# Optimization experiments

Measured on AMD Instinct MI355X. Metric: run time of the kernel, lower is better.

The kernel has to match this reference:

```python
import jax, jax.numpy as jnp
import numpy as np

B, S, D = 1, 4096, 512
H, DK, DV = 8, 64, 64


def setup_inputs() -> dict:
    key = jax.random.key(0)
    ks = jax.random.split(key, 8)
    s = 1.0 / np.sqrt(D)
    return {
        "queries": jax.random.normal(ks[0], (B, S, D), jnp.float32),
        "keys": jax.random.normal(ks[1], (B, S, D), jnp.float32),
        "values": jax.random.normal(ks[2], (B, S, D), jnp.float32),
        # Linear weights stored as [in, out] for x @ W
        "Wq": jax.random.normal(ks[3], (D, H * DK), jnp.float32) * s,
        "Wk": jax.random.normal(ks[4], (D, H * DK), jnp.float32) * s,
        "Wv": jax.random.normal(ks[5], (D, H * DV), jnp.float32) * s,
        "Wo": jax.random.normal(ks[6], (H * DV, D), jnp.float32) * s,
        "bo": jax.random.normal(ks[7], (D,), jnp.float32) * 0.02,
    }


def reference(queries, keys, values, Wq, Wk, Wv, Wo, bo):
    b, qlen = values.shape[0], queries.shape[1]
    q = (queries @ Wq).reshape(b, qlen, H, DK)
    k = (keys @ Wk).reshape(b, keys.shape[1], H, DK)
    v = (values @ Wv).reshape(b, values.shape[1], H, DV)
    scale = DK ** 0.5
    # naive full attention: materialize [b, h, sq, sk] scores
    scores = jnp.einsum("bqhd,bkhd->bhqk", q, k) / scale
    attn = jax.nn.softmax(scores, axis=-1)
    out = jnp.einsum("bhqk,bkhd->bqhd", attn, v).reshape(b, qlen, H * DV)
    out = out @ Wo + bo          # first fc_out
    out = out @ Wo + bo          # second fc_out (module applies it twice when not reversible)
    return out
```

## Files before the change

kernel.cpp:

```cpp
#include <hip/hip_runtime.h>

#define S_LEN  4096
#define DMODEL 512
#define NH     8
#define HD     64

typedef _Float16 f16x8 __attribute__((ext_vector_type(8)));
typedef _Float16 f16x4 __attribute__((ext_vector_type(4)));
typedef float    f32x4 __attribute__((ext_vector_type(4)));

static __device__ __forceinline__ unsigned short f2h(float x) {
  return __builtin_bit_cast(unsigned short, (_Float16)x);
}

__global__ __launch_bounds__(256) void wtrans_kernel(
    const float* __restrict__ w0, const float* __restrict__ w1,
    const float* __restrict__ w2, const float* __restrict__ w3,
    unsigned short* __restrict__ o0, unsigned short* __restrict__ o1,
    unsigned short* __restrict__ o2, unsigned short* __restrict__ o3,
    unsigned short* __restrict__ o3s)
{
  __shared__ unsigned short T[64 * 72];
  const float* W; unsigned short* O;
  switch (blockIdx.z) {
    case 0:  W = w0; O = o0; break;
    case 1:  W = w1; O = o1; break;
    case 2:  W = w2; O = o2; break;
    default: W = w3; O = o3; break;
  }
  const int tid = threadIdx.x;
  const int k0 = blockIdx.x * 64, n0 = blockIdx.y * 64;
  const int c4 = (tid & 15) * 4;
#pragma unroll
  for (int rp = 0; rp < 4; ++rp) {
    int r = rp * 16 + (tid >> 4);
    float4 x = *(const float4*)(W + (k0 + r) * DMODEL + n0 + c4);
    T[(c4 + 0) * 72 + r] = f2h(x.x);
    T[(c4 + 1) * 72 + r] = f2h(x.y);
    T[(c4 + 2) * 72 + r] = f2h(x.z);
    T[(c4 + 3) * 72 + r] = f2h(x.w);
    if (blockIdx.z == 3) {
      f16x4 st;
      st[0] = (_Float16)x.x; st[1] = (_Float16)x.y;
      st[2] = (_Float16)x.z; st[3] = (_Float16)x.w;
      *(f16x4*)&o3s[(k0 + r) * DMODEL + n0 + c4] = st;
    }
  }
  __syncthreads();
#pragma unroll
  for (int it = 0; it < 2; ++it) {
    int i = tid + it * 256;
    int nl = i >> 3, c = i & 7;
    *(f16x8*)&O[(n0 + nl) * DMODEL + k0 + c * 8] = *(const f16x8*)&T[nl * 72 + c * 8];
  }
}

__global__ __launch_bounds__(256) void gemm_kernel(
    const void* __restrict__ A0, const void* __restrict__ A1,
    const void* __restrict__ A2, const void* __restrict__ A3,
    const unsigned short* __restrict__ B0, const unsigned short* __restrict__ B1,
    const unsigned short* __restrict__ B2, const unsigned short* __restrict__ B3,
    void* __restrict__ C0, void* __restrict__ C1,
    void* __restrict__ C2, void* __restrict__ C3,
    const float* __restrict__ bias, unsigned short* __restrict__ vtg,
    const float* __restrict__ wo_f32, const float* __restrict__ bo_in,
    float* __restrict__ bo2_out,
    int a_fp32_mask, int c_fp32_mask)
{
  constexpr int K = DMODEL, N = DMODEL;
  __shared__ unsigned short As[64 * 32];
  __shared__ unsigned short Bs[64 * 32];
  const int z = blockIdx.z;
  if (z == 3 && blockIdx.x >= 8) {
    if (blockIdx.x < 16 && blockIdx.y == 0 && wo_f32) {
      int col = (blockIdx.x - 8) * 64 + (threadIdx.x & 63);
      float s = bo_in[col];
#pragma unroll 8
      for (int j = 0; j < DMODEL; ++j) s = fmaf(bo_in[j], wo_f32[j * DMODEL + col], s);
      bo2_out[col] = s;
    }
    return;
  }
  const void* Av; const unsigned short* Bt; void* Cv;
  switch (z) {
    case 0:  Av = A0; Bt = B0; Cv = C0; break;
    case 1:  Av = A1; Bt = B1; Cv = C1; break;
    case 2:  Av = A2; Bt = B2; Cv = C2; break;
    default: Av = A3; Bt = B3; Cv = C3; break;
  }
  const int a_fp32 = (a_fp32_mask >> z) & 1;
  const int c_fp32 = (c_fp32_mask >> z) & 1;
  const int tid  = threadIdx.x;
  const int lane = tid & 63;
  const int wid  = tid >> 6;
  const int quad = lane >> 4, l16 = lane & 15;
  const int m0 = blockIdx.x * 64, n0 = blockIdx.y * 64;
  const int wm = (wid >> 1) * 32, wn = (wid & 1) * 32;
  const int r  = tid >> 2, ck = (tid & 3) * 8;
  f32x4 acc[2][2] = {};

  for (int k0 = 0; k0 < K; k0 += 32) {
    __syncthreads();
    if (a_fp32) {
      const float* p = (const float*)Av + (m0 + r) * K + k0 + ck;
      float4 x = *(const float4*)p;
      float4 y = *(const float4*)(p + 4);
      f16x8 av;
      av[0] = (_Float16)x.x; av[1] = (_Float16)x.y;
      av[2] = (_Float16)x.z; av[3] = (_Float16)x.w;
      av[4] = (_Float16)y.x; av[5] = (_Float16)y.y;
      av[6] = (_Float16)y.z; av[7] = (_Float16)y.w;
      *(f16x8*)&As[r * 32 + ck] = av;
    } else {
      *(f16x8*)&As[r * 32 + ck] =
          *(const f16x8*)((const unsigned short*)Av + (m0 + r) * K + k0 + ck);
    }
    *(f16x8*)&Bs[r * 32 + ck] = *(const f16x8*)(Bt + (n0 + r) * K + k0 + ck);
    __syncthreads();

    f16x8 a0 = *(const f16x8*)&As[(wm + l16) * 32 + quad * 8];
    f16x8 a1 = *(const f16x8*)&As[(wm + 16 + l16) * 32 + quad * 8];
    f16x8 b0 = *(const f16x8*)&Bs[(wn + l16) * 32 + quad * 8];
    f16x8 b1 = *(const f16x8*)&Bs[(wn + 16 + l16) * 32 + quad * 8];
    acc[0][0] = __builtin_amdgcn_mfma_f32_16x16x32_f16(a0, b0, acc[0][0], 0, 0, 0);
    acc[0][1] = __builtin_amdgcn_mfma_f32_16x16x32_f16(a0, b1, acc[0][1], 0, 0, 0);
    acc[1][0] = __builtin_amdgcn_mfma_f32_16x16x32_f16(a1, b0, acc[1][0], 0, 0, 0);
    acc[1][1] = __builtin_amdgcn_mfma_f32_16x16x32_f16(a1, b1, acc[1][1], 0, 0, 0);
  }

  const int do_vt = (vtg != nullptr) && (z == 2);
#pragma unroll
  for (int mt = 0; mt < 2; ++mt)
#pragma unroll
    for (int nt = 0; nt < 2; ++nt) {
      int col = n0 + wn + nt * 16 + l16;
      float bv = bias ? bias[col] : 0.f;
#pragma unroll
      for (int g = 0; g < 4; ++g) {
        int row = m0 + wm + mt * 16 + quad * 4 + g;
        float val = acc[mt][nt][g] + bv;
        if (do_vt)        vtg[col * S_LEN + row] = f2h(val);
        else if (c_fp32)  ((float*)Cv)[row * N + col] = val;
        else              ((unsigned short*)Cv)[row * N + col] = f2h(val);
      }
    }
}

__global__ __launch_bounds__(256) void attn_kernel(
    const unsigned short* __restrict__ Qb, const unsigned short* __restrict__ Kb,
    const unsigned short* __restrict__ VtG,
    float* __restrict__ P0, unsigned short* __restrict__ P1,
    float* __restrict__ mp, float* __restrict__ lp)
{
  __shared__ unsigned short Ks[2][64 * 72];
  __shared__ unsigned short Vt[2 * 64 * 64];
  __shared__ float Msc[2][2][16];
  __shared__ float Lsc[2][2][16];

  const int tid  = threadIdx.x;
  const int lane = tid & 63;
  const int wid  = tid >> 6;
  const int qp   = wid & 1;
  const int kh   = wid >> 1;
  const int quad = lane >> 4, l16 = lane & 15;
  const int qb = blockIdx.x, h = blockIdx.y, z = blockIdx.z;
  const int hc = h * HD;
  const int qbase = qb * 64 + qp * 32;
  const int kz = z * 2048;

  f16x8 bq[2][2];
#pragma unroll
  for (int s = 0; s < 2; ++s) {
    int qrow = qbase + s * 16 + l16;
    bq[s][0] = *(const f16x8*)(Qb + qrow * DMODEL + hc + quad * 8);
    bq[s][1] = *(const f16x8*)(Qb + qrow * DMODEL + hc + 32 + quad * 8);
  }

  f32x4 o[2][4] = {};
  float m_run[2] = {-1e30f, -1e30f}, l_run[2] = {0.f, 0.f};

  f16x8 kreg[4], vreg[4];
#pragma unroll
  for (int it = 0; it < 4; ++it) {
    int s = it * 256 + tid;
    int khs = s >> 9, n = (s >> 3) & 63, c = s & 7;
    kreg[it] = *(const f16x8*)(Kb + (kz + khs * 1024 + n) * DMODEL + hc + c * 8);
    vreg[it] = *(const f16x8*)(VtG + (hc + n) * S_LEN + kz + khs * 1024 + c * 8);
  }

  for (int kbi = 0; kbi < 16; ++kbi) {
    __syncthreads();
#pragma unroll
    for (int it = 0; it < 4; ++it) {
      int s = it * 256 + tid;
      int khs = s >> 9, n = (s >> 3) & 63, c = s & 7;
      *(f16x8*)&Ks[khs][n * 72 + c * 8] = kreg[it];
      int vbase = (khs * 64 + n) * 16;
      int n15 = n & 15;
      f16x4 lo = __builtin_shufflevector(vreg[it], vreg[it], 0, 1, 2, 3);
      f16x4 hi = __builtin_shufflevector(vreg[it], vreg[it], 4, 5, 6, 7);
      *(f16x4*)&Vt[(vbase + ((2 * c) ^ n15)) * 4]     = lo;
      *(f16x4*)&Vt[(vbase + ((2 * c + 1) ^ n15)) * 4] = hi;
    }
    __syncthreads();

    if (kbi + 1 < 16) {
      int kb1 = (kbi + 1) * 64;
#pragma unroll
      for (int it = 0; it < 4; ++it) {
        int s = it * 256 + tid;
        int khs = s >> 9, n = (s >> 3) & 63, c = s & 7;
        kreg[it] = *(const f16x8*)(Kb + (kz + khs * 1024 + kb1 + n) * DMODEL + hc + c * 8);
        vreg[it] = *(const f16x8*)(VtG + (hc + n) * S_LEN + kz + khs * 1024 + kb1 + c * 8);
      }
    }

    f32x4 sT[2][4];
#pragma unroll
    for (int kt = 0; kt < 4; ++kt) {
      f16x8 ak0 = *(const f16x8*)&Ks[kh][(kt * 16 + l16) * 72 + quad * 8];
      f16x8 ak1 = *(const f16x8*)&Ks[kh][(kt * 16 + l16) * 72 + 32 + quad * 8];
#pragma unroll
      for (int s = 0; s < 2; ++s) {
        f32x4 a = {};
        a = __builtin_amdgcn_mfma_f32_16x16x32_f16(ak0, bq[s][0], a, 0, 0, 0);
        a = __builtin_amdgcn_mfma_f32_16x16x32_f16(ak1, bq[s][1], a, 0, 0, 0);
        sT[s][kt] = a;
      }
    }

    f16x4 pa[2][4];
#pragma unroll
    for (int s = 0; s < 2; ++s) {
      float vmax = -1e30f;
#pragma unroll
      for (int kt = 0; kt < 4; ++kt)
#pragma unroll
        for (int g = 0; g < 4; ++g) vmax = fmaxf(vmax, sT[s][kt][g]);
      vmax = fmaxf(vmax, __shfl_xor(vmax, 16));
      vmax = fmaxf(vmax, __shfl_xor(vmax, 32));

      if (__all(vmax <= m_run[s] + 8.0f)) {
        const float mn = m_run[s];
        float rs = 0.f;
#pragma unroll
        for (int kt = 0; kt < 4; ++kt)
#pragma unroll
          for (int g = 0; g < 4; ++g) {
            float p = __expf((sT[s][kt][g] - mn) * 0.125f);
            rs += p;
            pa[s][kt][g] = (_Float16)p;
          }
        rs += __shfl_xor(rs, 16);
        rs += __shfl_xor(rs, 32);
        l_run[s] += rs;
      } else {
        const float mn = fmaxf(m_run[s], vmax);
        const float alpha = __expf((m_run[s] - mn) * 0.125f);
        m_run[s] = mn;

        float rs = 0.f;
#pragma unroll
        for (int kt = 0; kt < 4; ++kt)
#pragma unroll
          for (int g = 0; g < 4; ++g) {
            float p = __expf((sT[s][kt][g] - mn) * 0.125f);
            rs += p;
            pa[s][kt][g] = (_Float16)p;
          }
        rs += __shfl_xor(rs, 16);
        rs += __shfl_xor(rs, 32);
        l_run[s] = l_run[s] * alpha + rs;

        float ag[4];
#pragma unroll
        for (int g = 0; g < 4; ++g) ag[g] = __shfl(alpha, quad * 4 + g);
#pragma unroll
        for (int nt = 0; nt < 4; ++nt)
#pragma unroll
          for (int g = 0; g < 4; ++g) o[s][nt][g] *= ag[g];
      }
    }

#pragma unroll
    for (int nt = 0; nt < 4; ++nt) {
      int dbase = (kh * 64 + nt * 16 + l16) * 16;
#pragma unroll
      for (int kt = 0; kt < 4; ++kt) {
        f16x4 bv = *(const f16x4*)&Vt[(dbase + ((kt * 4 + quad) ^ l16)) * 4];
#pragma unroll
        for (int s = 0; s < 2; ++s)
          o[s][nt] = __builtin_amdgcn_mfma_f32_16x16x16f16(pa[s][kt], bv, o[s][nt], 0, 0, 0);
      }
    }
  }

  __syncthreads();
  _Float16* Osc = (_Float16*)&Ks[0][0];
  if (kh == 1) {
#pragma unroll
    for (int s = 0; s < 2; ++s) {
      if (quad == 0) { Msc[qp][s][l16] = m_run[s]; Lsc[qp][s][l16] = l_run[s]; }
#pragma unroll
      for (int nt = 0; nt < 4; ++nt)
#pragma unroll
        for (int g = 0; g < 4; ++g)
          Osc[(qp * 64 + lane) * 32 + s * 16 + nt * 4 + g] = (_Float16)o[s][nt][g];
    }
  }
  __syncthreads();
  if (kh == 0) {
#pragma unroll
    for (int s = 0; s < 2; ++s) {
      const float m1 = Msc[qp][s][l16];
      const float l1 = Lsc[qp][s][l16];
      const float m  = fmaxf(m_run[s], m1);
      const float a0 = __expf((m_run[s] - m) * 0.125f);
      const float a1 = __expf((m1 - m) * 0.125f);
      const float lt = l_run[s] * a0 + l1 * a1;
      const float rl = 1.f / lt;
      if (quad == 0) {
        int q = qbase + s * 16 + l16;
        mp[(z * NH + h) * S_LEN + q] = m;
        lp[(z * NH + h) * S_LEN + q] = lt;
      }
      float a0g[4], a1g[4], rlg[4];
#pragma unroll
      for (int g = 0; g < 4; ++g) {
        a0g[g] = __shfl(a0, quad * 4 + g);
        a1g[g] = __shfl(a1, quad * 4 + g);
        rlg[g] = __shfl(rl, quad * 4 + g);
      }
#pragma unroll
      for (int g = 0; g < 4; ++g) {
        int row = qbase + s * 16 + quad * 4 + g;
#pragma unroll
        for (int nt = 0; nt < 4; ++nt) {
          float om = o[s][nt][g] * a0g[g] + (float)Osc[(qp * 64 + lane) * 32 + s * 16 + nt * 4 + g] * a1g[g];
          float val = om * rlg[g];
          if (z == 0) P0[row * DMODEL + hc + nt * 16 + l16] = val;
          else        P1[row * DMODEL + hc + nt * 16 + l16] = f2h(val);
        }
      }
    }
  }
}

__global__ __launch_bounds__(256) void merge_kernel(
    const float* __restrict__ P0, const unsigned short* __restrict__ P1,
    const float* __restrict__ mp, const float* __restrict__ lp,
    unsigned short* __restrict__ Ob)
{
  const int tid = threadIdx.x;
  const int qb = blockIdx.x, h = blockIdx.y;
  const int q = qb * 64 + (tid >> 2), hc = h * HD;
  const int dq = (tid & 3) * 16;
  const float m0 = mp[h * S_LEN + q],        l0 = lp[h * S_LEN + q];
  const float m1 = mp[(NH + h) * S_LEN + q], l1 = lp[(NH + h) * S_LEN + q];
  const float M  = fmaxf(m0, m1);
  float w0 = l0 * __expf((m0 - M) * 0.125f);
  float w1 = l1 * __expf((m1 - M) * 0.125f);
  const float rw = 1.f / (w0 + w1);
  w0 *= rw; w1 *= rw;
  const int base = q * DMODEL + hc + dq;
  f16x8 p1a = *(const f16x8*)&P1[base];
  f16x8 p1b = *(const f16x8*)&P1[base + 8];
  float4 x0 = *(const float4*)&P0[base];
  float4 x1 = *(const float4*)&P0[base + 4];
  float4 x2 = *(const float4*)&P0[base + 8];
  float4 x3 = *(const float4*)&P0[base + 12];
  f16x8 oa, ob;
  oa[0] = (_Float16)(w0 * x0.x + w1 * (float)p1a[0]);
  oa[1] = (_Float16)(w0 * x0.y + w1 * (float)p1a[1]);
  oa[2] = (_Float16)(w0 * x0.z + w1 * (float)p1a[2]);
  oa[3] = (_Float16)(w0 * x0.w + w1 * (float)p1a[3]);
  oa[4] = (_Float16)(w0 * x1.x + w1 * (float)p1a[4]);
  oa[5] = (_Float16)(w0 * x1.y + w1 * (float)p1a[5]);
  oa[6] = (_Float16)(w0 * x1.z + w1 * (float)p1a[6]);
  oa[7] = (_Float16)(w0 * x1.w + w1 * (float)p1a[7]);
  ob[0] = (_Float16)(w0 * x2.x + w1 * (float)p1b[0]);
  ob[1] = (_Float16)(w0 * x2.y + w1 * (float)p1b[1]);
  ob[2] = (_Float16)(w0 * x2.z + w1 * (float)p1b[2]);
  ob[3] = (_Float16)(w0 * x2.w + w1 * (float)p1b[3]);
  ob[4] = (_Float16)(w0 * x3.x + w1 * (float)p1b[4]);
  ob[5] = (_Float16)(w0 * x3.y + w1 * (float)p1b[5]);
  ob[6] = (_Float16)(w0 * x3.z + w1 * (float)p1b[6]);
  ob[7] = (_Float16)(w0 * x3.w + w1 * (float)p1b[7]);
  *(f16x8*)&Ob[base]     = oa;
  *(f16x8*)&Ob[base + 8] = ob;
}

extern "C" void kernel_launch(void* const* d_in, const int* in_sizes, int n_in,
                              void* d_out, int out_size, void* d_ws, size_t ws_size,
                              hipStream_t stream) {
  const float* q  = (const float*)d_in[0];
  const float* k  = (const float*)d_in[1];
  const float* v  = (const float*)d_in[2];
  const float* Wq = (const float*)d_in[3];
  const float* Wk = (const float*)d_in[4];
  const float* Wv = (const float*)d_in[5];
  const float* Wo = (const float*)d_in[6];
  const float* bo = (const float*)d_in[7];

  unsigned short* ws   = (unsigned short*)d_ws;
  unsigned short* Wqt  = ws;
  unsigned short* Wkt  = Wqt  + 262144;
  unsigned short* Wvt  = Wkt  + 262144;
  unsigned short* Wot  = Wvt  + 262144;
  unsigned short* Wof  = Wot  + 262144;
  unsigned short* Wo2t = Wof  + 262144;
  unsigned short* Qb   = Wo2t + 262144;
  unsigned short* Kb   = Qb   + 2097152;
  unsigned short* VtG  = Kb   + 2097152;
  unsigned short* Ab   = VtG  + 2097152;
  float*          bo2  = (float*)(Ab + 2097152);
  float*          mp   = bo2 + 512;
  float*          lp   = mp + 65536;

  wtrans_kernel<<<dim3(8, 8, 4), 256, 0, stream>>>(
      Wq, Wk, Wv, Wo, Wqt, Wkt, Wvt, Wot, Wof);

  gemm_kernel<<<dim3(64, 8, 4), 256, 0, stream>>>(
      q, k, v, Wot, Wqt, Wkt, Wvt, Wof, Qb, Kb, nullptr, Wo2t,
      nullptr, VtG, Wo, bo, bo2, 0x7, 0x0);

  attn_kernel<<<dim3(64, 8, 2), 256, 0, stream>>>(
      Qb, Kb, VtG, (float*)d_out, Ab, mp, lp);

  merge_kernel<<<dim3(64, 8), 256, 0, stream>>>(
      (const float*)d_out, Ab, mp, lp, Ab);

  gemm_kernel<<<dim3(64, 8, 1), 256, 0, stream>>>(
      Ab, nullptr, nullptr, nullptr, Wo2t, nullptr, nullptr, nullptr,
      d_out, nullptr, nullptr, nullptr, bo2, nullptr,
      nullptr, nullptr, nullptr, 0x0, 0x1);
}
```

Measured before the change: 213.6 us.

## Enlarge GEMM tiles to 128x128 and register-prefetch next K slice

The projection and output GEMMs move from 64x64 to 128x128 block tiles, with each wave computing a 4x4 grid of 16x16 MFMA tiles instead of 2x2. Global loads for the next K slice are issued into registers before the current slice's MFMAs, so memory latency overlaps with compute. This raises reuse of each shared-memory fragment and cuts redundant global reads. In exchange it uses more registers and launches far fewer blocks (128 per projection, 128 for the final GEMM), which may underfill the GPU's compute units.

```diff
diff --git a/kernel.cpp b/kernel.cpp
--- a/kernel.cpp
+++ b/kernel.cpp
@@ -55,7 +55,7 @@
   }
 }
 
-__global__ __launch_bounds__(256) void gemm_kernel(
+__global__ __launch_bounds__(256) void gemm128_kernel(
     const void* __restrict__ A0, const void* __restrict__ A1,
     const void* __restrict__ A2, const void* __restrict__ A3,
     const unsigned short* __restrict__ B0, const unsigned short* __restrict__ B1,
@@ -68,12 +68,12 @@
     int a_fp32_mask, int c_fp32_mask)
 {
   constexpr int K = DMODEL, N = DMODEL;
-  __shared__ unsigned short As[64 * 32];
-  __shared__ unsigned short Bs[64 * 32];
+  __shared__ unsigned short As[128 * 32];
+  __shared__ unsigned short Bs[128 * 32];
   const int z = blockIdx.z;
-  if (z == 3 && blockIdx.x >= 8) {
-    if (blockIdx.x < 16 && blockIdx.y == 0 && wo_f32) {
-      int col = (blockIdx.x - 8) * 64 + (threadIdx.x & 63);
+  if (z == 3 && blockIdx.x >= 4) {
+    if (blockIdx.x < 12 && blockIdx.y == 0 && wo_f32) {
+      int col = (blockIdx.x - 4) * 64 + (threadIdx.x & 63);
       float s = bo_in[col];
 #pragma unroll 8
       for (int j = 0; j < DMODEL; ++j) s = fmaf(bo_in[j], wo_f32[j * DMODEL + col], s);
@@ -94,15 +94,17 @@
   const int lane = tid & 63;
   const int wid  = tid >> 6;
   const int quad = lane >> 4, l16 = lane & 15;
-  const int m0 = blockIdx.x * 64, n0 = blockIdx.y * 64;
-  const int wm = (wid >> 1) * 32, wn = (wid & 1) * 32;
-  const int r  = tid >> 2, ck = (tid & 3) * 8;
-  f32x4 acc[2][2] = {};
-
-  for (int k0 = 0; k0 < K; k0 += 32) {
-    __syncthreads();
+  const int m0 = blockIdx.x * 128, n0 = blockIdx.y * 128;
+  const int wm = (wid >> 1) * 64, wn = (wid & 1) * 64;
+  f32x4 acc[4][4] = {};
+
+  f16x8 areg[2], breg[2];
+#pragma unroll
+  for (int it = 0; it < 2; ++it) {
+    int s = it * 256 + tid;
+    int r = s >> 2, ck = (s & 3) * 8;
     if (a_fp32) {
-      const float* p = (const float*)Av + (m0 + r) * K + k0 + ck;
+      const float* p = (const float*)Av + (m0 + r) * K + ck;
       float4 x = *(const float4*)p;
       float4 y = *(const float4*)(p + 4);
       f16x8 av;
@@ -110,29 +112,66 @@
       av[2] = (_Float16)x.z; av[3] = (_Float16)x.w;
       av[4] = (_Float16)y.x; av[5] = (_Float16)y.y;
       av[6] = (_Float16)y.z; av[7] = (_Float16)y.w;
-      *(f16x8*)&As[r * 32 + ck] = av;
+      areg[it] = av;
     } else {
-      *(f16x8*)&As[r * 32 + ck] =
-          *(const f16x8*)((const unsigned short*)Av + (m0 + r) * K + k0 + ck);
-    }
-    *(f16x8*)&Bs[r * 32 + ck] = *(const f16x8*)(Bt + (n0 + r) * K + k0 + ck);
+      areg[it] = *(const f16x8*)((const unsigned short*)Av + (m0 + r) * K + ck);
+    }
+    breg[it] = *(const f16x8*)(Bt + (n0 + r) * K + ck);
+  }
+
+  for (int k0 = 0; k0 < K; k0 += 32) {
     __syncthreads();
-
-    f16x8 a0 = *(const f16x8*)&As[(wm + l16) * 32 + quad * 8];
-    f16x8 a1 = *(const f16x8*)&As[(wm + 16 + l16) * 32 + quad * 8];
-    f16x8 b0 = *(const f16x8*)&Bs[(wn + l16) * 32 + quad * 8];
-    f16x8 b1 = *(const f16x8*)&Bs[(wn + 16 + l16) * 32 + quad * 8];
-    acc[0][0] = __builtin_amdgcn_mfma_f32_16x16x32_f16(a0, b0, acc[0][0], 0, 0, 0);
-    acc[0][1] = __builtin_amdgcn_mfma_f32_16x16x32_f16(a0, b1, acc[0][1], 0, 0, 0);
-    acc[1][0] = __builtin_amdgcn_mfma_f32_16x16x32_f16(a1, b0, acc[1][0], 0, 0, 0);
-    acc[1][1] = __builtin_amdgcn_mfma_f32_16x16x32_f16(a1, b1, acc[1][1], 0, 0, 0);
+#pragma unroll
+    for (int it = 0; it < 2; ++it) {
+      int s = it * 256 + tid;
+      int r = s >> 2, ck = (s & 3) * 8;
+      *(f16x8*)&As[r * 32 + ck] = areg[it];
+      *(f16x8*)&Bs[r * 32 + ck] = breg[it];
+    }
+    __syncthreads();
+
+    if (k0 + 32 < K) {
+      int kk = k0 + 32;
+#pragma unroll
+      for (int it = 0; it < 2; ++it) {
+        int s = it * 256 + tid;
+        int r = s >> 2, ck = (s & 3) * 8;
+        if (a_fp32) {
+          const float* p = (const float*)Av + (m0 + r) * K + kk + ck;
+          float4 x = *(const float4*)p;
+          float4 y = *(const float4*)(p + 4);
+          f16x8 av;
+          av[0] = (_Float16)x.x; av[1] = (_Float16)x.y;
+          av[2] = (_Float16)x.z; av[3] = (_Float16)x.w;
+          av[4] = (_Float16)y.x; av[5] = (_Float16)y.y;
+          av[6] = (_Float16)y.z; av[7] = (_Float16)y.w;
+          areg[it] = av;
+        } else {
+          areg[it] = *(const f16x8*)((const unsigned short*)Av + (m0 + r) * K + kk + ck);
+        }
+        breg[it] = *(const f16x8*)(Bt + (n0 + r) * K + kk + ck);
+      }
+    }
+
+    f16x8 af[4], bf[4];
+#pragma unroll
+    for (int mt = 0; mt < 4; ++mt)
+      af[mt] = *(const f16x8*)&As[(wm + mt * 16 + l16) * 32 + quad * 8];
+#pragma unroll
+    for (int nt = 0; nt < 4; ++nt)
+      bf[nt] = *(const f16x8*)&Bs[(wn + nt * 16 + l16) * 32 + quad * 8];
+#pragma unroll
+    for (int mt = 0; mt < 4; ++mt)
+#pragma unroll
+      for (int nt = 0; nt < 4; ++nt)
+        acc[mt][nt] = __builtin_amdgcn_mfma_f32_16x16x32_f16(af[mt], bf[nt], acc[mt][nt], 0, 0, 0);
   }
 
   const int do_vt = (vtg != nullptr) && (z == 2);
 #pragma unroll
-  for (int mt = 0; mt < 2; ++mt)
-#pragma unroll
-    for (int nt = 0; nt < 2; ++nt) {
+  for (int mt = 0; mt < 4; ++mt)
+#pragma unroll
+    for (int nt = 0; nt < 4; ++nt) {
       int col = n0 + wn + nt * 16 + l16;
       float bv = bias ? bias[col] : 0.f;
 #pragma unroll
@@ -420,7 +459,7 @@
   wtrans_kernel<<<dim3(8, 8, 4), 256, 0, stream>>>(
       Wq, Wk, Wv, Wo, Wqt, Wkt, Wvt, Wot, Wof);
 
-  gemm_kernel<<<dim3(64, 8, 4), 256, 0, stream>>>(
+  gemm128_kernel<<<dim3(32, 4, 4), 256, 0, stream>>>(
       q, k, v, Wot, Wqt, Wkt, Wvt, Wof, Qb, Kb, nullptr, Wo2t,
       nullptr, VtG, Wo, bo, bo2, 0x7, 0x0);
 
@@ -430,7 +469,7 @@
   merge_kernel<<<dim3(64, 8), 256, 0, stream>>>(
       (const float*)d_out, Ab, mp, lp, Ab);
 
-  gemm_kernel<<<dim3(64, 8, 1), 256, 0, stream>>>(
+  gemm128_kernel<<<dim3(32, 4, 1), 256, 0, stream>>>(
       Ab, nullptr, nullptr, nullptr, Wo2t, nullptr, nullptr, nullptr,
       d_out, nullptr, nullptr, nullptr, bo2, nullptr,
       nullptr, nullptr, nullptr, 0x0, 0x1);
```

After: 212.9 us. Within noise of the previous version (-0.3%).
